# Optimization experiments

Hardware: AMD Instinct MI355X
Metric: run time of the kernel (lower is better)

Reference implementation:

```python
import jax, jax.numpy as jnp
import numpy as np

N_NODES = 50000
N_EDGES = 800000
IN_DIM = 256
OUT_DIM = 64
HEADS = 4
NEG_SLOPE = 0.2  # PyG GATConv default


def setup_inputs() -> dict:
    key = jax.random.key(0)
    k1, k2, k3, k4, k5, k6 = jax.random.split(key, 6)
    x = jax.random.normal(k1, (N_NODES, IN_DIM), dtype=jnp.float32)
    edge_index = jax.random.randint(k2, (2, N_EDGES), 0, N_NODES, dtype=jnp.int64)
    scale = 1.0 / np.sqrt(IN_DIM)
    W = jax.random.normal(k3, (IN_DIM, HEADS * OUT_DIM), dtype=jnp.float32) * scale
    att_src = jax.random.normal(k4, (HEADS, OUT_DIM), dtype=jnp.float32) * scale
    att_dst = jax.random.normal(k5, (HEADS, OUT_DIM), dtype=jnp.float32) * scale
    bias = jnp.zeros((HEADS * OUT_DIM,), dtype=jnp.float32)
    return {"x": x, "edge_index": edge_index, "W": W,
            "att_src": att_src, "att_dst": att_dst, "bias": bias}


def reference(x, edge_index, W, att_src, att_dst, bias):
    N = x.shape[0]
    H, C = att_src.shape
    # add self loops (PyG GATConv default add_self_loops=True)
    loop = jnp.arange(N, dtype=edge_index.dtype)
    src = jnp.concatenate([edge_index[0], loop])  # [E+N] source j
    dst = jnp.concatenate([edge_index[1], loop])  # [E+N] target i
    # linear projection, per-head features  [N, H, C]
    h = (x @ W).reshape(N, H, C)
    # attention logits: a_src . h_j + a_dst . h_i  -> [E, H]
    a_src = jnp.einsum('nhc,hc->nh', h, att_src)
    a_dst = jnp.einsum('nhc,hc->nh', h, att_dst)
    e = jax.nn.leaky_relu(a_src[src] + a_dst[dst], negative_slope=NEG_SLOPE)
    # edge softmax over incoming edges of each destination node
    m = jax.ops.segment_max(e, dst, num_segments=N)          # [N, H]
    p = jnp.exp(e - m[dst])                                  # [E, H]
    denom = jax.ops.segment_sum(p, dst, num_segments=N)      # [N, H]
    alpha = p / (denom[dst] + 1e-16)                         # [E, H]
    # weighted scatter-aggregate of gathered source features
    out = jax.ops.segment_sum(alpha[:, :, None] * h[src], dst, num_segments=N)
    out = out.reshape(N, H * C) + bias
    return jax.nn.relu(out)  # GATLayer active_func
```

## Files before the change

kernel.cpp:

```cpp
#include <hip/hip_runtime.h>

constexpr int N  = 50000;
constexpr int E  = 800000;
constexpr int K  = 256;
constexpr int F  = 256;
constexpr int H  = 4;
constexpr float SLOPE = 0.2f;

constexpr int CAPS = 6;

constexpr int NBK  = 98;
constexpr int BCAP = 16384;
constexpr int BKB  = 256;
constexpr int EPB  = E / BKB;

constexpr int WT_ROWS = 272;

constexpr size_t OFF_HB   = 0;
constexpr size_t OFF_WT   = OFF_HB   + (size_t)N * F * 2;
constexpr size_t OFF_ASRC = OFF_WT   + (size_t)WT_ROWS * K * 2;
constexpr size_t OFF_ADST = OFF_ASRC + (size_t)N * H * 4;
constexpr size_t OFF_DEG  = OFF_ADST + (size_t)N * H * 4;
constexpr size_t OFF_FLAG = OFF_DEG  + (size_t)N * 4;
constexpr size_t OFF_CSR  = OFF_FLAG + 64;
constexpr size_t OFF_BUF  = OFF_CSR  + (size_t)N * 64 * 4;
constexpr size_t OFF_GCUR = OFF_BUF  + (size_t)NBK * BCAP * 4;

constexpr int GEMM_TILES  = (N + 63) / 64;
constexpr int GEMM_BLOCKS = GEMM_TILES * 2;

typedef short short8 __attribute__((ext_vector_type(8)));
typedef float floatx4 __attribute__((ext_vector_type(4)));

__device__ __forceinline__ float leaky(float x) {
    return x > 0.f ? x : SLOPE * x;
}
__device__ __forceinline__ float blo(unsigned u) { return __uint_as_float(u << 16); }
__device__ __forceinline__ float bhi(unsigned u) { return __uint_as_float(u & 0xffff0000u); }
__device__ __forceinline__ unsigned short f2b(float f) {
    unsigned u = __float_as_uint(f);
    return (unsigned short)((u + 0x7fffu + ((u >> 16) & 1u)) >> 16);
}
__device__ __forceinline__ unsigned pk2(float a, float b) {
    return (unsigned)f2b(a) | ((unsigned)f2b(b) << 16);
}

__device__ __forceinline__ int edge_at(const void* ei, int is64, size_t i) {
    if (is64) return (int)((const long long*)ei)[i];
    return ((const int*)ei)[i];
}

__global__ __launch_bounds__(256)
void prep(const float* __restrict__ Wm, const float* __restrict__ att_src,
          const float* __restrict__ att_dst, const unsigned* __restrict__ ei_words,
          unsigned short* __restrict__ Wt, int* __restrict__ flag,
          int* __restrict__ gcur) {
    __shared__ float tile[64][65];
    __shared__ float as_l[64], ad_l[64];
    const int bid = blockIdx.x;
    const int t = threadIdx.x;
    if (bid < 16) {
        const int k0 = (bid & 3) * 64;
        const int n0 = (bid >> 2) * 64;
        const int r = t >> 2;
        const int c4 = (t & 3) * 16;
        #pragma unroll
        for (int i = 0; i < 16; i += 4) {
            float4 v = *reinterpret_cast<const float4*>(
                Wm + (size_t)(k0 + r) * F + n0 + c4 + i);
            tile[r][c4 + i + 0] = v.x;
            tile[r][c4 + i + 1] = v.y;
            tile[r][c4 + i + 2] = v.z;
            tile[r][c4 + i + 3] = v.w;
        }
        __syncthreads();
        unsigned pk[8];
        #pragma unroll
        for (int j = 0; j < 8; ++j)
            pk[j] = pk2(tile[c4 + 2 * j + 0][r], tile[c4 + 2 * j + 1][r]);
        unsigned short* dst = Wt + (size_t)(n0 + r) * K + k0 + c4;
        *reinterpret_cast<uint4*>(dst)     = make_uint4(pk[0], pk[1], pk[2], pk[3]);
        *reinterpret_cast<uint4*>(dst + 8) = make_uint4(pk[4], pk[5], pk[6], pk[7]);
    } else if (bid < 20) {
        const int h = bid - 16;
        if (t < 64) {
            as_l[t] = att_src[h * 64 + t];
            ad_l[t] = att_dst[h * 64 + t];
        }
        __syncthreads();
        const int k = t;
        const float* wr = Wm + (size_t)k * F + h * 64;
        float s = 0.f, d = 0.f;
        #pragma unroll
        for (int c = 0; c < 64; c += 4) {
            float4 w = *reinterpret_cast<const float4*>(wr + c);
            s += w.x * as_l[c] + w.y * as_l[c + 1]
               + w.z * as_l[c + 2] + w.w * as_l[c + 3];
            d += w.x * ad_l[c] + w.y * ad_l[c + 1]
               + w.z * ad_l[c + 2] + w.w * ad_l[c + 3];
        }
        Wt[(size_t)(256 + h) * K + k] = f2b(s);
        Wt[(size_t)(260 + h) * K + k] = f2b(d);
        if (h == 0) {
            #pragma unroll
            for (int r = 0; r < 8; ++r) Wt[(size_t)(264 + r) * K + k] = 0;
        }
    } else {
        if (t < 64) {
            unsigned v = ei_words[2 * t + 1];
            unsigned long long b = __ballot(v != 0u);
            if (t == 0) *flag = (b == 0ull) ? 1 : 0;
        }
        for (int j = t; j < NBK * 16; j += 256) gcur[j] = 0;
    }
}

constexpr int LDA = 72;
constexpr int LDW = 72;

__global__ __launch_bounds__(256, 5)
void gemm_hist(const float* __restrict__ X, const unsigned short* __restrict__ Wt,
               unsigned short* __restrict__ Hb, float* __restrict__ asrc,
               float* __restrict__ adst, const void* __restrict__ ei,
               const int* __restrict__ flag, unsigned* __restrict__ buf,
               int* __restrict__ gcur) {
    __shared__ unsigned short Al[64 * LDA];
    __shared__ unsigned short Wl[144 * LDW];
    const int tid = threadIdx.x;

    if (blockIdx.x < BKB) {
        int* cnt = (int*)(void*)Al;
        int* gsh = cnt + 128;
        int* scn = gsh + 128;
        unsigned* staged = (unsigned*)(void*)Wl;
        const int is64 = *flag;
        const int e0 = blockIdx.x * EPB;
        if (tid < 128) cnt[tid] = 0;
        __syncthreads();
        for (int it = 0; it < (EPB + 255) / 256; ++it) {
            int idx = it * 256 + tid;
            if (idx < EPB) {
                int d = edge_at(ei, is64, (size_t)E + e0 + idx);
                atomicAdd(&cnt[d >> 9], 1);
            }
        }
        __syncthreads();
        if (tid < 128) scn[tid] = cnt[tid];
        __syncthreads();
        for (int off = 1; off < 128; off <<= 1) {
            int v = 0;
            if (tid < 128 && tid >= off) v = scn[tid - off];
            __syncthreads();
            if (tid < 128) scn[tid] += v;
            __syncthreads();
        }
        if (tid < 128) {
            int c = cnt[tid];
            int lbase = scn[tid] - c;
            int gb = 0;
            if (c > 0 && tid < NBK) gb = atomicAdd(&gcur[tid * 16], c);
            gsh[tid] = gb - lbase;
            cnt[tid] = lbase;
        }
        __syncthreads();
        for (int it = 0; it < (EPB + 255) / 256; ++it) {
            int idx = it * 256 + tid;
            if (idx < EPB) {
                int d = edge_at(ei, is64, (size_t)E + e0 + idx);
                int s = edge_at(ei, is64, (size_t)(e0 + idx));
                int bk = d >> 9;
                int slot = atomicAdd(&cnt[bk], 1);
                staged[slot] = ((unsigned)bk << 25)
                             | ((unsigned)(d & 511) << 16) | (unsigned)s;
            }
        }
        __syncthreads();
        for (int j = tid; j < EPB; j += 256) {
            unsigned v = staged[j];
            int bk = (int)(v >> 25);
            buf[(size_t)bk * BCAP + gsh[bk] + j] = v;
        }
        return;
    }

    const int bid = blockIdx.x - BKB;
    const int tileR = bid >> 1;
    const int halfC = bid & 1;
    const int m0 = tileR * 64;
    const int c0 = halfC * 128;

    const int wv = tid >> 6, lane = tid & 63;
    const int quad = lane >> 4, l15 = lane & 15;
    const bool fusedw = (halfC == 1) && (wv == 3);

    floatx4 acc[4][2];
    #pragma unroll
    for (int i = 0; i < 4; ++i)
        #pragma unroll
        for (int j = 0; j < 2; ++j) acc[i][j] = (floatx4)0.f;
    floatx4 accf[4];
    #pragma unroll
    for (int i = 0; i < 4; ++i) accf[i] = (floatx4)0.f;

    const int ar = tid >> 2;
    const int akc = (tid & 3) * 16;
    const bool arow_ok = (m0 + ar) < N;
    const int wr = tid >> 1;
    const int wkc = (tid & 1) * 32;

    for (int k0 = 0; k0 < K; k0 += 64) {
        {
            const float* src = X + (size_t)(m0 + ar) * K + k0 + akc;
            unsigned short* dst = &Al[ar * LDA + akc];
            #pragma unroll
            for (int i = 0; i < 16; i += 4) {
                float4 v = arow_ok ? *reinterpret_cast<const float4*>(src + i)
                                   : make_float4(0.f, 0.f, 0.f, 0.f);
                *reinterpret_cast<uint2*>(dst + i) =
                    make_uint2(pk2(v.x, v.y), pk2(v.z, v.w));
            }
        }
        {
            const unsigned short* src = Wt + (size_t)(c0 + wr) * K + k0 + wkc;
            unsigned short* dst = &Wl[wr * LDW + wkc];
            #pragma unroll
            for (int i = 0; i < 32; i += 8)
                *reinterpret_cast<int4*>(dst + i) =
                    *reinterpret_cast<const int4*>(src + i);
        }
        if (halfC == 1 && tid < 64) {
            const int fr = tid >> 2;
            const int fk = (tid & 3) * 16;
            const unsigned short* src = Wt + (size_t)(256 + fr) * K + k0 + fk;
            unsigned short* dst = &Wl[(128 + fr) * LDW + fk];
            *reinterpret_cast<int4*>(dst)     = *reinterpret_cast<const int4*>(src);
            *reinterpret_cast<int4*>(dst + 8) = *reinterpret_cast<const int4*>(src + 8);
        }
        __syncthreads();
        #pragma unroll
        for (int kk = 0; kk < 64; kk += 32) {
            short8 a[4];
            #pragma unroll
            for (int i = 0; i < 4; ++i)
                a[i] = *reinterpret_cast<const short8*>(
                    &Al[(i * 16 + l15) * LDA + kk + quad * 8]);
            #pragma unroll
            for (int j = 0; j < 2; ++j) {
                short8 b = *reinterpret_cast<const short8*>(
                    &Wl[(wv * 32 + j * 16 + l15) * LDW + kk + quad * 8]);
                #pragma unroll
                for (int i = 0; i < 4; ++i)
                    acc[i][j] = __builtin_amdgcn_mfma_f32_16x16x32_bf16(
                        a[i], b, acc[i][j], 0, 0, 0);
            }
            if (fusedw) {
                short8 bf = *reinterpret_cast<const short8*>(
                    &Wl[(128 + l15) * LDW + kk + quad * 8]);
                #pragma unroll
                for (int i = 0; i < 4; ++i)
                    accf[i] = __builtin_amdgcn_mfma_f32_16x16x32_bf16(
                        a[i], bf, accf[i], 0, 0, 0);
            }
        }
        __syncthreads();
    }
    #pragma unroll
    for (int i = 0; i < 4; ++i) {
        const int row = m0 + i * 16 + quad * 4;
        #pragma unroll
        for (int j = 0; j < 2; ++j) {
            const int colb = c0 + wv * 32 + j * 16;
            #pragma unroll
            for (int r = 0; r < 4; ++r) {
                float v = acc[i][j][r];
                float vn = __shfl_xor(v, 1);
                unsigned p = pk2(v, vn);
                unsigned q = __shfl_xor(p, 2);
                if ((l15 & 3) == 0 && (row + r) < N) {
                    *reinterpret_cast<uint2*>(
                        &Hb[(size_t)(row + r) * F + colb + l15]) =
                        make_uint2(p, q);
                }
            }
        }
    }
    if (fusedw) {
        #pragma unroll
        for (int i = 0; i < 4; ++i) {
            const int rbase = m0 + i * 16 + quad * 4;
            #pragma unroll
            for (int r = 0; r < 4; ++r) {
                int row = rbase + r;
                if (row < N) {
                    if (l15 < 4)      asrc[row * H + l15] = accf[i][r];
                    else if (l15 < 8) adst[row * H + (l15 - 4)] = accf[i][r];
                }
            }
        }
    }
}

__global__ __launch_bounds__(256)
void rank_scatter(const unsigned* __restrict__ buf, const int* __restrict__ gcur,
                  int* __restrict__ csr, int* __restrict__ deg) {
    __shared__ int h[512];
    const int b = blockIdx.x;
    const int t = threadIdx.x;
    h[t] = 0; h[t + 256] = 0;
    __syncthreads();
    const int nb = gcur[b * 16];
    for (int j = t; j < nb; j += 256) {
        unsigned v = buf[(size_t)b * BCAP + j];
        int dl = (int)((v >> 16) & 511u);
        int s  = (int)(v & 0xffffu);
        int r = atomicAdd(&h[dl], 1);
        csr[(((b << 9) + dl) << CAPS) + r] = s;
    }
    __syncthreads();
    int n0 = (b << 9) + t;
    if (n0 < N) deg[n0] = h[t];
    if (n0 + 256 < N) deg[n0 + 256] = h[t + 256];
}

__global__ __launch_bounds__(256, 8)
void aggregate(const unsigned short* __restrict__ Hb, const float* __restrict__ asrc,
               const float* __restrict__ adst, const int* __restrict__ deg,
               const int* __restrict__ csr, const float* __restrict__ bias,
               float* __restrict__ out) {
    const int wv = threadIdx.x >> 6;
    const int lane = threadIdx.x & 63;
    const int half = lane >> 5;
    const int l32 = lane & 31;
    const int hd = l32 >> 3;
    const int node = blockIdx.x * 4 + wv;

    const char* hbase = (const char*)Hb;
    const char* abase = (const char*)asrc;
    const unsigned lsh = (unsigned)l32 << 4;
    const unsigned hsh = (unsigned)hd << 2;

    const float adsti = adst[node * H + hd];
    const int start = node << CAPS;
    const int end = start + deg[node];

    float denom = 0.f;
    float a0 = 0.f, a1 = 0.f, a2 = 0.f, a3 = 0.f;
    float a4 = 0.f, a5 = 0.f, a6 = 0.f, a7 = 0.f;
    int e = start;
    for (; e + 8 <= end; e += 8) {
        unsigned s[4]; float l[4]; uint4 u[4];
        #pragma unroll
        for (int j = 0; j < 4; ++j) s[j] = (unsigned)csr[e + 2 * j + half];
        #pragma unroll
        for (int j = 0; j < 4; ++j)
            l[j] = *(const float*)(abase + ((s[j] << 4) + hsh));
        #pragma unroll
        for (int j = 0; j < 4; ++j)
            u[j] = *(const uint4*)(hbase + ((s[j] << 9) + lsh));
        #pragma unroll
        for (int j = 0; j < 4; ++j) {
            float p = __expf(leaky(l[j] + adsti));
            denom += p;
            a0 += p * blo(u[j].x); a1 += p * bhi(u[j].x);
            a2 += p * blo(u[j].y); a3 += p * bhi(u[j].y);
            a4 += p * blo(u[j].z); a5 += p * bhi(u[j].z);
            a6 += p * blo(u[j].w); a7 += p * bhi(u[j].w);
        }
    }
    for (; e + 2 <= end; e += 2) {
        unsigned s0 = (unsigned)csr[e + half];
        float l0 = *(const float*)(abase + ((s0 << 4) + hsh));
        uint4 u0 = *(const uint4*)(hbase + ((s0 << 9) + lsh));
        float p = __expf(leaky(l0 + adsti));
        denom += p;
        a0 += p * blo(u0.x); a1 += p * bhi(u0.x);
        a2 += p * blo(u0.y); a3 += p * bhi(u0.y);
        a4 += p * blo(u0.z); a5 += p * bhi(u0.z);
        a6 += p * blo(u0.w); a7 += p * bhi(u0.w);
    }
    {
        const int rem = end - e;
        bool active;
        unsigned sf;
        if (half == 0) { active = (rem == 1); sf = active ? (unsigned)csr[e] : 0u; }
        else           { active = true;       sf = (unsigned)node; }
        if (active) {
            float l0 = *(const float*)(abase + ((sf << 4) + hsh));
            uint4 u0 = *(const uint4*)(hbase + ((sf << 9) + lsh));
            float p = __expf(leaky(l0 + adsti));
            denom += p;
            a0 += p * blo(u0.x); a1 += p * bhi(u0.x);
            a2 += p * blo(u0.y); a3 += p * bhi(u0.y);
            a4 += p * blo(u0.z); a5 += p * bhi(u0.z);
            a6 += p * blo(u0.w); a7 += p * bhi(u0.w);
        }
    }
    a0 += __shfl_xor(a0, 32); a1 += __shfl_xor(a1, 32);
    a2 += __shfl_xor(a2, 32); a3 += __shfl_xor(a3, 32);
    a4 += __shfl_xor(a4, 32); a5 += __shfl_xor(a5, 32);
    a6 += __shfl_xor(a6, 32); a7 += __shfl_xor(a7, 32);
    denom += __shfl_xor(denom, 32);
    if (half == 0) {
        const float inv = 1.f / (denom + 1e-16f);
        float4 b0 = *reinterpret_cast<const float4*>(bias + l32 * 8);
        float4 b1 = *reinterpret_cast<const float4*>(bias + l32 * 8 + 4);
        float4 o0, o1;
        o0.x = fmaxf(a0 * inv + b0.x, 0.f);
        o0.y = fmaxf(a1 * inv + b0.y, 0.f);
        o0.z = fmaxf(a2 * inv + b0.z, 0.f);
        o0.w = fmaxf(a3 * inv + b0.w, 0.f);
        o1.x = fmaxf(a4 * inv + b1.x, 0.f);
        o1.y = fmaxf(a5 * inv + b1.y, 0.f);
        o1.z = fmaxf(a6 * inv + b1.z, 0.f);
        o1.w = fmaxf(a7 * inv + b1.w, 0.f);
        float* orow = out + (size_t)node * F + l32 * 8;
        *reinterpret_cast<float4*>(orow)     = o0;
        *reinterpret_cast<float4*>(orow + 4) = o1;
    }
}

extern "C" void kernel_launch(void* const* d_in, const int* in_sizes, int n_in,
                              void* d_out, int out_size, void* d_ws, size_t ws_size,
                              hipStream_t stream) {
    const float* x       = (const float*)d_in[0];
    const void*  ei      = d_in[1];
    const float* Wm      = (const float*)d_in[2];
    const float* att_src = (const float*)d_in[3];
    const float* att_dst = (const float*)d_in[4];
    const float* bias    = (const float*)d_in[5];
    float* out = (float*)d_out;

    char* ws = (char*)d_ws;
    unsigned short* hb = (unsigned short*)(ws + OFF_HB);
    unsigned short* wt = (unsigned short*)(ws + OFF_WT);
    float* asrc = (float*)(ws + OFF_ASRC);
    float* adst = (float*)(ws + OFF_ADST);
    int* deg  = (int*)(ws + OFF_DEG);
    int* flag = (int*)(ws + OFF_FLAG);
    int* csr  = (int*)(ws + OFF_CSR);
    unsigned* buf = (unsigned*)(ws + OFF_BUF);
    int* gcur = (int*)(ws + OFF_GCUR);

    prep<<<21, 256, 0, stream>>>(Wm, att_src, att_dst, (const unsigned*)ei,
                                 wt, flag, gcur);
    gemm_hist<<<BKB + GEMM_BLOCKS, 256, 0, stream>>>(
        x, wt, hb, asrc, adst, ei, flag, buf, gcur);
    rank_scatter<<<NBK, 256, 0, stream>>>(buf, gcur, csr, deg);
    aggregate<<<N / 4, 256, 0, stream>>>(hb, asrc, adst, deg, csr, bias, out);
}
```

Measured before the change: 221.2 us.

## Slice projected features into 32-column panels and aggregate per slice for cache locality

The GEMM now writes the bf16 features in a sliced layout: 8 panels of 32 columns, each stored as [N,32]. The aggregate kernel is restructured so that each block handles one column slice for 32 nodes. Each 8-lane group processes one node and gathers 8-byte chunks, which shrinks the randomly gathered working set per slice so it fits in cache better. In exchange, the CSR indices and attention logits are re-read once per slice, and the exp is recomputed 8 times per edge. Separately, rank_scatter now uses 1024 threads per block and leaky ReLU is written as fmaxf.

```diff
diff --git a/kernel.cpp b/kernel.cpp
--- a/kernel.cpp
+++ b/kernel.cpp
@@ -29,11 +29,14 @@
 constexpr int GEMM_TILES  = (N + 63) / 64;
 constexpr int GEMM_BLOCKS = GEMM_TILES * 2;
 
+constexpr int AGG_GROUPS = (N + 31) / 32;
+constexpr int AGG_BLOCKS = AGG_GROUPS * 8;
+
 typedef short short8 __attribute__((ext_vector_type(8)));
 typedef float floatx4 __attribute__((ext_vector_type(4)));
 
 __device__ __forceinline__ float leaky(float x) {
-    return x > 0.f ? x : SLOPE * x;
+    return fmaxf(x, SLOPE * x);
 }
 __device__ __forceinline__ float blo(unsigned u) { return __uint_as_float(u << 16); }
 __device__ __forceinline__ float bhi(unsigned u) { return __uint_as_float(u & 0xffff0000u); }
@@ -277,8 +280,10 @@
                 unsigned p = pk2(v, vn);
                 unsigned q = __shfl_xor(p, 2);
                 if ((l15 & 3) == 0 && (row + r) < N) {
+                    const int c = colb + l15;
+                    const int sl = c >> 5;
                     *reinterpret_cast<uint2*>(
-                        &Hb[(size_t)(row + r) * F + colb + l15]) =
+                        &Hb[((size_t)sl * N + (row + r)) * 32 + (c & 31)]) =
                         make_uint2(p, q);
                 }
             }
@@ -300,16 +305,16 @@
     }
 }
 
-__global__ __launch_bounds__(256)
+__global__ __launch_bounds__(1024)
 void rank_scatter(const unsigned* __restrict__ buf, const int* __restrict__ gcur,
                   int* __restrict__ csr, int* __restrict__ deg) {
     __shared__ int h[512];
     const int b = blockIdx.x;
     const int t = threadIdx.x;
-    h[t] = 0; h[t + 256] = 0;
+    if (t < 512) h[t] = 0;
     __syncthreads();
     const int nb = gcur[b * 16];
-    for (int j = t; j < nb; j += 256) {
+    for (int j = t; j < nb; j += 1024) {
         unsigned v = buf[(size_t)b * BCAP + j];
         int dl = (int)((v >> 16) & 511u);
         int s  = (int)(v & 0xffffu);
@@ -317,9 +322,10 @@
         csr[(((b << 9) + dl) << CAPS) + r] = s;
     }
     __syncthreads();
-    int n0 = (b << 9) + t;
-    if (n0 < N) deg[n0] = h[t];
-    if (n0 + 256 < N) deg[n0 + 256] = h[t + 256];
+    if (t < 512) {
+        int n0 = (b << 9) + t;
+        if (n0 < N) deg[n0] = h[t];
+    }
 }
 
 __global__ __launch_bounds__(256, 8)
@@ -327,95 +333,51 @@
                const float* __restrict__ adst, const int* __restrict__ deg,
                const int* __restrict__ csr, const float* __restrict__ bias,
                float* __restrict__ out) {
-    const int wv = threadIdx.x >> 6;
-    const int lane = threadIdx.x & 63;
-    const int half = lane >> 5;
-    const int l32 = lane & 31;
-    const int hd = l32 >> 3;
-    const int node = blockIdx.x * 4 + wv;
-
-    const char* hbase = (const char*)Hb;
-    const char* abase = (const char*)asrc;
-    const unsigned lsh = (unsigned)l32 << 4;
-    const unsigned hsh = (unsigned)hd << 2;
-
-    const float adsti = adst[node * H + hd];
+    const int tid = threadIdx.x;
+    const int wv = tid >> 6;
+    const int lane = tid & 63;
+    const int gr = lane >> 3;
+    const int l8 = lane & 7;
+    const int sl = blockIdx.x & 7;
+    const int node = (blockIdx.x >> 3) * 32 + wv * 8 + gr;
+    const int hd = sl >> 1;
+    const bool nok = node < N;
+
+    const char* pbase = (const char*)Hb + (size_t)sl * N * 64;
+    const unsigned coff = (unsigned)(l8 << 3);
+
+    const float adsti = nok ? adst[node * H + hd] : 0.f;
     const int start = node << CAPS;
-    const int end = start + deg[node];
-
-    float denom = 0.f;
-    float a0 = 0.f, a1 = 0.f, a2 = 0.f, a3 = 0.f;
-    float a4 = 0.f, a5 = 0.f, a6 = 0.f, a7 = 0.f;
-    int e = start;
-    for (; e + 8 <= end; e += 8) {
-        unsigned s[4]; float l[4]; uint4 u[4];
-        #pragma unroll
-        for (int j = 0; j < 4; ++j) s[j] = (unsigned)csr[e + 2 * j + half];
-        #pragma unroll
-        for (int j = 0; j < 4; ++j)
-            l[j] = *(const float*)(abase + ((s[j] << 4) + hsh));
-        #pragma unroll
-        for (int j = 0; j < 4; ++j)
-            u[j] = *(const uint4*)(hbase + ((s[j] << 9) + lsh));
-        #pragma unroll
-        for (int j = 0; j < 4; ++j) {
-            float p = __expf(leaky(l[j] + adsti));
-            denom += p;
-            a0 += p * blo(u[j].x); a1 += p * bhi(u[j].x);
-            a2 += p * blo(u[j].y); a3 += p * bhi(u[j].y);
-            a4 += p * blo(u[j].z); a5 += p * bhi(u[j].z);
-            a6 += p * blo(u[j].w); a7 += p * bhi(u[j].w);
-        }
-    }
-    for (; e + 2 <= end; e += 2) {
-        unsigned s0 = (unsigned)csr[e + half];
-        float l0 = *(const float*)(abase + ((s0 << 4) + hsh));
-        uint4 u0 = *(const uint4*)(hbase + ((s0 << 9) + lsh));
-        float p = __expf(leaky(l0 + adsti));
-        denom += p;
-        a0 += p * blo(u0.x); a1 += p * bhi(u0.x);
-        a2 += p * blo(u0.y); a3 += p * bhi(u0.y);
-        a4 += p * blo(u0.z); a5 += p * bhi(u0.z);
-        a6 += p * blo(u0.w); a7 += p * bhi(u0.w);
-    }
-    {
-        const int rem = end - e;
-        bool active;
-        unsigned sf;
-        if (half == 0) { active = (rem == 1); sf = active ? (unsigned)csr[e] : 0u; }
-        else           { active = true;       sf = (unsigned)node; }
-        if (active) {
-            float l0 = *(const float*)(abase + ((sf << 4) + hsh));
-            uint4 u0 = *(const uint4*)(hbase + ((sf << 9) + lsh));
-            float p = __expf(leaky(l0 + adsti));
-            denom += p;
-            a0 += p * blo(u0.x); a1 += p * bhi(u0.x);
-            a2 += p * blo(u0.y); a3 += p * bhi(u0.y);
-            a4 += p * blo(u0.z); a5 += p * bhi(u0.z);
-            a6 += p * blo(u0.w); a7 += p * bhi(u0.w);
-        }
-    }
-    a0 += __shfl_xor(a0, 32); a1 += __shfl_xor(a1, 32);
-    a2 += __shfl_xor(a2, 32); a3 += __shfl_xor(a3, 32);
-    a4 += __shfl_xor(a4, 32); a5 += __shfl_xor(a5, 32);
-    a6 += __shfl_xor(a6, 32); a7 += __shfl_xor(a7, 32);
-    denom += __shfl_xor(denom, 32);
-    if (half == 0) {
+    const int dg = nok ? deg[node] : -1;
+    const int cnt = dg + 1;
+
+    float denom = 0.f, a0 = 0.f, a1 = 0.f, a2 = 0.f, a3 = 0.f;
+    for (int e = 0; e < cnt; e += 2) {
+        uint2 c2 = *reinterpret_cast<const uint2*>(&csr[start + e]);
+        unsigned s0 = (e < dg) ? c2.x : (unsigned)node;
+        bool e1 = (e + 1) < cnt;
+        unsigned s1 = ((e + 1) < dg) ? c2.y : (unsigned)node;
+        float l0 = asrc[s0 * H + hd];
+        float l1 = asrc[s1 * H + hd];
+        uint2 u0 = *(const uint2*)(pbase + ((s0 << 6) + coff));
+        uint2 u1 = *(const uint2*)(pbase + ((s1 << 6) + coff));
+        float p0 = __expf(leaky(l0 + adsti));
+        float p1 = e1 ? __expf(leaky(l1 + adsti)) : 0.f;
+        denom += p0 + p1;
+        a0 += p0 * blo(u0.x) + p1 * blo(u1.x);
+        a1 += p0 * bhi(u0.x) + p1 * bhi(u1.x);
+        a2 += p0 * blo(u0.y) + p1 * blo(u1.y);
+        a3 += p0 * bhi(u0.y) + p1 * bhi(u1.y);
+    }
+    if (nok) {
         const float inv = 1.f / (denom + 1e-16f);
-        float4 b0 = *reinterpret_cast<const float4*>(bias + l32 * 8);
-        float4 b1 = *reinterpret_cast<const float4*>(bias + l32 * 8 + 4);
-        float4 o0, o1;
-        o0.x = fmaxf(a0 * inv + b0.x, 0.f);
-        o0.y = fmaxf(a1 * inv + b0.y, 0.f);
-        o0.z = fmaxf(a2 * inv + b0.z, 0.f);
-        o0.w = fmaxf(a3 * inv + b0.w, 0.f);
-        o1.x = fmaxf(a4 * inv + b1.x, 0.f);
-        o1.y = fmaxf(a5 * inv + b1.y, 0.f);
-        o1.z = fmaxf(a6 * inv + b1.z, 0.f);
-        o1.w = fmaxf(a7 * inv + b1.w, 0.f);
-        float* orow = out + (size_t)node * F + l32 * 8;
-        *reinterpret_cast<float4*>(orow)     = o0;
-        *reinterpret_cast<float4*>(orow + 4) = o1;
+        float4 bv = *reinterpret_cast<const float4*>(bias + sl * 32 + l8 * 4);
+        float4 o;
+        o.x = fmaxf(a0 * inv + bv.x, 0.f);
+        o.y = fmaxf(a1 * inv + bv.y, 0.f);
+        o.z = fmaxf(a2 * inv + bv.z, 0.f);
+        o.w = fmaxf(a3 * inv + bv.w, 0.f);
+        *reinterpret_cast<float4*>(out + (size_t)node * F + sl * 32 + l8 * 4) = o;
     }
 }
 
@@ -445,6 +407,6 @@
                                  wt, flag, gcur);
     gemm_hist<<<BKB + GEMM_BLOCKS, 256, 0, stream>>>(
         x, wt, hb, asrc, adst, ei, flag, buf, gcur);
-    rank_scatter<<<NBK, 256, 0, stream>>>(buf, gcur, csr, deg);
-    aggregate<<<N / 4, 256, 0, stream>>>(hb, asrc, adst, deg, csr, bias, out);
-}
+    rank_scatter<<<NBK, 1024, 0, stream>>>(buf, gcur, csr, deg);
+    aggregate<<<AGG_BLOCKS, 256, 0, stream>>>(hb, asrc, adst, deg, csr, bias, out);
+}
```

Result: slower. 249.2 us (+12.7%).
